# Kernel tuning notes

Measured on AMD Instinct MI355X. Metric: run time of the kernel, lower is better.

The kernel has to match this reference:

```python
import jax, jax.numpy as jnp
import numpy as np

B, OBS, D, V = 32, 768, 512, 64  # batch, obs_dim, latent/action/embed dim, max_vars


def _gelu(x):
    return jax.nn.gelu(x, approximate=False)  # torch nn.GELU default is exact erf


def setup_inputs() -> dict:
    key = jax.random.key(0)
    ks = jax.random.split(key, 16)
    s = lambda k, shape, scale=0.02: (jax.random.normal(k, shape, jnp.float32) * scale)
    return {
        "obs": jax.random.normal(ks[0], (B, OBS), jnp.float32),
        "action": jax.random.normal(ks[1], (B, D), jnp.float32),
        # CausalGraphLearner params
        "embed": jax.random.normal(ks[2], (V, D), jnp.float32),  # nn.Embedding weight
        "sc_w1": s(ks[3], (2 * D, 3 * D)), "sc_b1": jnp.zeros((2 * D,), jnp.float32),
        "sc_w2": s(ks[4], (1, 2 * D)), "sc_b2": jnp.zeros((1,), jnp.float32),
        # WorldModelEngine params
        "enc_w1": s(ks[5], (2 * D, OBS)), "enc_b1": jnp.zeros((2 * D,), jnp.float32),
        "enc_w2": s(ks[6], (D, 2 * D)), "enc_b2": jnp.zeros((D,), jnp.float32),
        "gru_wih": s(ks[7], (3 * D, 2 * D)), "gru_whh": s(ks[8], (3 * D, D)),
        "gru_bih": jnp.zeros((3 * D,), jnp.float32), "gru_bhh": jnp.zeros((3 * D,), jnp.float32),
        "dec_w": s(ks[9], (OBS, D)), "dec_b": jnp.zeros((OBS,), jnp.float32),
        # reasoner params
        "rs_w1": s(ks[10], (D, D)), "rs_b1": jnp.zeros((D,), jnp.float32),
        "rs_w2": s(ks[11], (D, D)), "rs_b2": jnp.zeros((D,), jnp.float32),
    }


def reference(obs, action, embed, sc_w1, sc_b1, sc_w2, sc_b2,
              enc_w1, enc_b1, enc_w2, enc_b2,
              gru_wih, gru_whh, gru_bih, gru_bhh,
              dec_w, dec_b, rs_w1, rs_b1, rs_w2, rs_b2):
    # --- WorldModelEngine ---
    z = _gelu(obs @ enc_w1.T + enc_b1) @ enc_w2.T + enc_b2            # [B, D]
    x = jnp.concatenate([z, action], axis=-1)                          # [B, 2D]
    h0 = jnp.zeros((obs.shape[0], D), obs.dtype)                       # h=None -> zeros
    gi = x @ gru_wih.T + gru_bih                                       # [B, 3D]
    gh = h0 @ gru_whh.T + gru_bhh                                      # [B, 3D]
    r = jax.nn.sigmoid(gi[:, :D] + gh[:, :D])
    u = jax.nn.sigmoid(gi[:, D:2 * D] + gh[:, D:2 * D])
    n = jnp.tanh(gi[:, 2 * D:] + r * gh[:, 2 * D:])
    h = (1.0 - u) * n + u * h0                                         # [B, D]
    pred = h @ dec_w.T + dec_b                                         # [B, OBS]

    # --- CausalGraphLearner ---
    # Linear-of-concat identity: W1 @ cat(cause, effect, ctx) = Wa@cause + Wb@effect + Wc@ctx
    Wa, Wb, Wc = sc_w1[:, :D], sc_w1[:, D:2 * D], sc_w1[:, 2 * D:]
    Ea = embed @ Wa.T                                                  # [V, 2D]
    Eb = embed @ Wb.T                                                  # [V, 2D]
    Cc = (h + action) @ Wc.T                                           # [B, 2D]
    hid = _gelu(Cc[:, None, None, :] + Ea[None, :, None, :]
                + Eb[None, None, :, :] + sc_b1)                        # [B, V, V, 2D]
    scores = jax.nn.sigmoid(jnp.einsum('bijd,d->bij', hid, sc_w2[0]) + sc_b2[0])  # [B,V,V]
    graph = scores.mean(0)                                             # [V, V] (returned scores)

    # --- reasoner ---
    reasoning = _gelu(h @ rs_w1.T + rs_b1) @ rs_w2.T + rs_b2           # [B, D]

    return (h, pred, graph, reasoning)
```

## Files before the change

### kernel.cpp

```cpp
#include <hip/hip_runtime.h>
#include <math.h>


#if __has_builtin(__builtin_amdgcn_exp2f)
#define EXP2F __builtin_amdgcn_exp2f
#else
#define EXP2F exp2f
#endif

typedef float f32x2 __attribute__((ext_vector_type(2)));

__device__ __forceinline__ float gelu_exact(float x) {
    return 0.5f * x * (1.f + erff(x * 0.70710678118654752f));
}
__device__ __forceinline__ float sigmoid_fast(float v) {
    return __builtin_amdgcn_rcpf(1.f + EXP2F(-1.442695041f * v));
}
__device__ __forceinline__ float tanh_fast(float v) {
    return fmaf(-2.f, __builtin_amdgcn_rcpf(1.f + EXP2F(2.885390082f * v)), 1.f);
}

template<int NF4, int ACT, int BT>
__device__ __forceinline__ void wgemm(int wid,
        const float* __restrict__ A, int lda,
        const float* __restrict__ W, int ldw,
        const float* __restrict__ bias,
        float* __restrict__ out, int ldo,
        int oblocks) {
    int lane = threadIdx.x & 63;
    int oblock = wid % oblocks;
    int bgroup = wid / oblocks;
    int o0 = oblock * 8, b0 = bgroup * BT;

    float4 w[8][NF4];
#pragma unroll
    for (int r = 0; r < 8; ++r) {
        const float4* wr = reinterpret_cast<const float4*>(W + (o0 + r) * ldw);
#pragma unroll
        for (int c = 0; c < NF4; ++c) w[r][c] = wr[c * 64 + lane];
    }
#pragma unroll 2
    for (int bi = 0; bi < BT; ++bi) {
        const float4* ar = reinterpret_cast<const float4*>(A + (b0 + bi) * lda);
        float4 a[NF4];
#pragma unroll
        for (int c = 0; c < NF4; ++c) a[c] = ar[c * 64 + lane];
        float s[8];
#pragma unroll
        for (int r = 0; r < 8; ++r) {
            float acc = 0.f;
#pragma unroll
            for (int c = 0; c < NF4; ++c) {
                acc = fmaf(a[c].x, w[r][c].x, acc);
                acc = fmaf(a[c].y, w[r][c].y, acc);
                acc = fmaf(a[c].z, w[r][c].z, acc);
                acc = fmaf(a[c].w, w[r][c].w, acc);
            }
            s[r] = acc;
        }
#pragma unroll
        for (int m = 1; m < 64; m <<= 1) {
#pragma unroll
            for (int r = 0; r < 8; ++r) s[r] += __shfl_xor(s[r], m, 64);
        }
        if (lane == 0) {
#pragma unroll
            for (int r = 0; r < 8; ++r) {
                float v = s[r] + (bias ? bias[o0 + r] : 0.f);
                if (ACT) v = gelu_exact(v);
                out[(b0 + bi) * ldo + o0 + r] = v;
            }
        }
    }
}

__global__ void __launch_bounds__(256) front_kernel(
    const float* __restrict__ obs, const float* __restrict__ enc_w1,
    const float* __restrict__ enc_b1, float* __restrict__ h1,
    const float* __restrict__ embed, const float* __restrict__ sc_w1,
    const float* __restrict__ sc_b1, float* __restrict__ Ea, float* __restrict__ Eb,
    const float* __restrict__ action, const float* __restrict__ wih,
    const float* __restrict__ bih, float* __restrict__ gia) {
    int wid = blockIdx.x * 4 + (threadIdx.x >> 6);
    if (wid < 512) {
        wgemm<3, 1, 8>(wid, obs, 768, enc_w1, 768, enc_b1, h1, 1024, 128);
    } else if (wid < 1536) {
        wgemm<2, 0, 8>(wid - 512, embed, 512, sc_w1, 1536, sc_b1, Ea, 1024, 128);
    } else if (wid < 2560) {
        wgemm<2, 0, 8>(wid - 1536, embed, 512, sc_w1 + 512, 1536, nullptr, Eb, 1024, 128);
    } else {
        wgemm<2, 0, 8>(wid - 2560, action, 512, wih + 512, 1024, bih, gia, 1536, 192);
    }
}

__global__ void __launch_bounds__(256) enc2_kernel(
    const float* __restrict__ h1, const float* __restrict__ enc_w2,
    const float* __restrict__ enc_b2, float* __restrict__ z) {
    int wid = blockIdx.x * 4 + (threadIdx.x >> 6);
    wgemm<4, 0, 4>(wid, h1, 1024, enc_w2, 1024, enc_b2, z, 512, 64);
}

__global__ void __launch_bounds__(256) gigru_kernel(
    const float* __restrict__ z, const float* __restrict__ wih,
    const float* __restrict__ gia, const float* __restrict__ bhh,
    const float* __restrict__ action, float* __restrict__ h, float* __restrict__ ha) {
    int wid = blockIdx.x * 4 + (threadIdx.x >> 6);
    int lane = threadIdx.x & 63;
    int opair = wid & 255;
    int bg = wid >> 8;
    int o0 = opair * 2, b0 = bg * 4;

    int rows[6] = {o0, o0 + 1, 512 + o0, 513 + o0, 1024 + o0, 1025 + o0};
    float4 w[6][2];
#pragma unroll
    for (int r = 0; r < 6; ++r) {
        const float4* wr = reinterpret_cast<const float4*>(wih + rows[r] * 1024);
#pragma unroll
        for (int c = 0; c < 2; ++c) w[r][c] = wr[c * 64 + lane];
    }
    float bhr0 = bhh[o0],        bhr1 = bhh[o0 + 1];
    float bhu0 = bhh[512 + o0],  bhu1 = bhh[513 + o0];
    float bhn0 = bhh[1024 + o0], bhn1 = bhh[1025 + o0];

#pragma unroll 2
    for (int bi = 0; bi < 4; ++bi) {
        int b = b0 + bi;
        const float4* ar = reinterpret_cast<const float4*>(z + b * 512);
        float4 a[2] = {ar[lane], ar[64 + lane]};
        float s[6];
#pragma unroll
        for (int r = 0; r < 6; ++r) {
            float acc = 0.f;
#pragma unroll
            for (int c = 0; c < 2; ++c) {
                acc = fmaf(a[c].x, w[r][c].x, acc);
                acc = fmaf(a[c].y, w[r][c].y, acc);
                acc = fmaf(a[c].z, w[r][c].z, acc);
                acc = fmaf(a[c].w, w[r][c].w, acc);
            }
            s[r] = acc;
        }
#pragma unroll
        for (int m = 1; m < 64; m <<= 1) {
#pragma unroll
            for (int r = 0; r < 6; ++r) s[r] += __shfl_xor(s[r], m, 64);
        }
        if (lane == 0) {
            const float* gb = gia + b * 1536;
            float r0 = sigmoid_fast(s[0] + gb[o0]        + bhr0);
            float r1 = sigmoid_fast(s[1] + gb[o0 + 1]    + bhr1);
            float u0 = sigmoid_fast(s[2] + gb[512 + o0]  + bhu0);
            float u1 = sigmoid_fast(s[3] + gb[513 + o0]  + bhu1);
            float n0 = tanh_fast(s[4] + gb[1024 + o0] + r0 * bhn0);
            float n1 = tanh_fast(s[5] + gb[1025 + o0] + r1 * bhn1);
            float hv0 = (1.f - u0) * n0;
            float hv1 = (1.f - u1) * n1;
            h[b * 512 + o0]      = hv0;
            h[b * 512 + o0 + 1]  = hv1;
            ha[b * 512 + o0]     = hv0 + action[b * 512 + o0];
            ha[b * 512 + o0 + 1] = hv1 + action[b * 512 + o0 + 1];
        }
    }
}

__global__ void __launch_bounds__(256) mid_kernel(
    const float* __restrict__ h, const float* __restrict__ ha,
    const float* __restrict__ dec_w, const float* __restrict__ dec_b, float* __restrict__ pred,
    const float* __restrict__ rs_w1, const float* __restrict__ rs_b1, float* __restrict__ r1,
    const float* __restrict__ sc_w1, float* __restrict__ Cc) {
    int wid = blockIdx.x * 4 + (threadIdx.x >> 6);
    if (wid < 768) {
        wgemm<2, 0, 4>(wid, h, 512, dec_w, 512, dec_b, pred, 768, 96);
    } else if (wid < 1280) {
        wgemm<2, 1, 4>(wid - 768, h, 512, rs_w1, 512, rs_b1, r1, 512, 64);
    } else {
        wgemm<2, 0, 4>(wid - 1280, ha, 512, sc_w1 + 1024, 1536, nullptr, Cc, 1024, 128);
    }
}

__global__ void __launch_bounds__(256) score_rs2_kernel(
    const float* __restrict__ Ea, const float* __restrict__ Eb,
    const float* __restrict__ Cc, const float* __restrict__ w2,
    const float* __restrict__ b2, float* __restrict__ graph,
    const float* __restrict__ r1, const float* __restrict__ rs_w2,
    const float* __restrict__ rs_b2, float* __restrict__ reasoning) {
    int blk = blockIdx.x;
    if (blk < 64) {
        int wid = blk * 4 + (threadIdx.x >> 6);
        wgemm<2, 0, 8>(wid, r1, 512, rs_w2, 512, rs_b2, reasoning, 512, 64);
    }
    int i = blk >> 5;
    int j0 = (blk & 31) << 1;
    int lane = threadIdx.x & 63;
    int wave = threadIdx.x >> 6;
    int d0 = lane << 4;

    const float4* Ea4  = reinterpret_cast<const float4*>(Ea + i * 1024 + d0);
    const float4* Eb04 = reinterpret_cast<const float4*>(Eb + j0 * 1024 + d0);
    const float4* Eb14 = reinterpret_cast<const float4*>(Eb + (j0 + 1) * 1024 + d0);
    const float4* W4   = reinterpret_cast<const float4*>(w2 + d0);

    f32x2 basea[8], baseb[8], wv[8];
#pragma unroll
    for (int c = 0; c < 4; ++c) {
        float4 e  = Ea4[c];
        float4 f0 = Eb04[c];
        float4 f1 = Eb14[c];
        float4 w  = W4[c];
        basea[2 * c]     = f32x2{e.x + f0.x, e.y + f0.y};
        basea[2 * c + 1] = f32x2{e.z + f0.z, e.w + f0.w};
        baseb[2 * c]     = f32x2{e.x + f1.x, e.y + f1.y};
        baseb[2 * c + 1] = f32x2{e.z + f1.z, e.w + f1.w};
        wv[2 * c]        = f32x2{w.x, w.y};
        wv[2 * c + 1]    = f32x2{w.z, w.w};
    }

    const f32x2 nk2  = f32x2{-2.4554274f, -2.4554274f};
    const f32x2 one2 = f32x2{1.f, 1.f};
    float bsc = b2[0];
    float gsum0 = 0.f, gsum1 = 0.f;
    const float4* p = reinterpret_cast<const float4*>(Cc + d0 + (wave * 8) * 1024);
    float4 m0 = p[0], m1 = p[1], m2 = p[2], m3 = p[3];

    for (int r = 0; r < 8; ++r) {
        f32x2 cc[8];
        cc[0] = f32x2{m0.x, m0.y}; cc[1] = f32x2{m0.z, m0.w};
        cc[2] = f32x2{m1.x, m1.y}; cc[3] = f32x2{m1.z, m1.w};
        cc[4] = f32x2{m2.x, m2.y}; cc[5] = f32x2{m2.z, m2.w};
        cc[6] = f32x2{m3.x, m3.y}; cc[7] = f32x2{m3.z, m3.w};
        if (r < 7) {
            const float4* q = reinterpret_cast<const float4*>(Cc + (wave * 8 + r + 1) * 1024 + d0);
            m0 = q[0]; m1 = q[1]; m2 = q[2]; m3 = q[3];
        }
        float s0 = 0.f, s1 = 0.f;
#pragma unroll
        for (int e = 0; e < 8; ++e) {
            f32x2 xA = cc[e] + basea[e];
            f32x2 xB = cc[e] + baseb[e];
            f32x2 aA = xA * nk2;
            f32x2 aB = xB * nk2;
            f32x2 tA, tB;
            tA.x = EXP2F(aA.x); tA.y = EXP2F(aA.y);
            tB.x = EXP2F(aB.x); tB.y = EXP2F(aB.y);
            f32x2 dA = tA + one2;
            f32x2 dB = tB + one2;
            f32x2 pA = xA * wv[e];
            f32x2 pB = xB * wv[e];
            float numA = fmaf(pA.x, dA.y, pA.y * dA.x);
            float numB = fmaf(pB.x, dB.y, pB.y * dB.x);
            float rrA = __builtin_amdgcn_rcpf(dA.x * dA.y);
            float rrB = __builtin_amdgcn_rcpf(dB.x * dB.y);
            s0 = fmaf(numA, rrA, s0);
            s1 = fmaf(numB, rrB, s1);
        }
#pragma unroll
        for (int m = 32; m >= 1; m >>= 1) {
            s0 += __shfl_xor(s0, m, 64);
            s1 += __shfl_xor(s1, m, 64);
        }
        if (lane == 0) {
            gsum0 += sigmoid_fast(s0 + bsc);
            gsum1 += sigmoid_fast(s1 + bsc);
        }
    }

    __shared__ float red[4][2];
    if (lane == 0) { red[wave][0] = gsum0; red[wave][1] = gsum1; }
    __syncthreads();
    if (threadIdx.x == 0) {
        graph[i * 64 + j0]     = (red[0][0] + red[1][0] + red[2][0] + red[3][0]) * 0.03125f;
        graph[i * 64 + j0 + 1] = (red[0][1] + red[1][1] + red[2][1] + red[3][1]) * 0.03125f;
    }
}

extern "C" void kernel_launch(void* const* d_in, const int* in_sizes, int n_in,
                              void* d_out, int out_size, void* d_ws, size_t ws_size,
                              hipStream_t stream) {
    const float* obs     = (const float*)d_in[0];
    const float* action  = (const float*)d_in[1];
    const float* embed   = (const float*)d_in[2];
    const float* sc_w1   = (const float*)d_in[3];
    const float* sc_b1   = (const float*)d_in[4];
    const float* sc_w2   = (const float*)d_in[5];
    const float* sc_b2   = (const float*)d_in[6];
    const float* enc_w1  = (const float*)d_in[7];
    const float* enc_b1  = (const float*)d_in[8];
    const float* enc_w2  = (const float*)d_in[9];
    const float* enc_b2  = (const float*)d_in[10];
    const float* gru_wih = (const float*)d_in[11];
    const float* gru_bih = (const float*)d_in[13];
    const float* gru_bhh = (const float*)d_in[14];
    const float* dec_w   = (const float*)d_in[15];
    const float* dec_b   = (const float*)d_in[16];
    const float* rs_w1   = (const float*)d_in[17];
    const float* rs_b1   = (const float*)d_in[18];
    const float* rs_w2   = (const float*)d_in[19];
    const float* rs_b2   = (const float*)d_in[20];

    float* ws = (float*)d_ws;
    float* h1  = ws + 0;
    float* z   = ws + 32768;
    float* gia = ws + 49152;
    float* ha  = ws + 98304;
    float* r1  = ws + 114688;
    float* Cc  = ws + 131072;
    float* Ea  = ws + 163840;
    float* Eb  = ws + 229376;

    float* h_out     = (float*)d_out;
    float* pred      = h_out + 16384;
    float* graph     = h_out + 40960;
    float* reasoning = h_out + 45056;

    front_kernel<<<832, 256, 0, stream>>>(obs, enc_w1, enc_b1, h1,
                                          embed, sc_w1, sc_b1, Ea, Eb,
                                          action, gru_wih, gru_bih, gia);
    enc2_kernel<<<128, 256, 0, stream>>>(h1, enc_w2, enc_b2, z);
    gigru_kernel<<<512, 256, 0, stream>>>(z, gru_wih, gia, gru_bhh, action, h_out, ha);
    mid_kernel<<<576, 256, 0, stream>>>(h_out, ha, dec_w, dec_b, pred,
                                        rs_w1, rs_b1, r1, sc_w1, Cc);
    score_rs2_kernel<<<2048, 256, 0, stream>>>(Ea, Eb, Cc, sc_w2, sc_b2, graph,
                                               r1, rs_w2, rs_b2, reasoning);
}
```

Measured before the change: 198.9 us.

## Use transpose-style shuffle reductions and halve batch tiles for more waves

The wave-level reductions in the GEMV helper and the score kernel now use a butterfly that folds several partial sums per shuffle step. This replaces independent full 64-lane reductions for each output and cuts the number of cross-lane shuffles. The score kernel now accumulates all 8 batch rows before a single combined reduction, instead of reducing once per row. The enc2, GRU and mid kernels use half the batch rows per wave with twice as many blocks, trading more weight reloads for more parallelism.

```diff
diff --git a/kernel.cpp b/kernel.cpp
--- a/kernel.cpp
+++ b/kernel.cpp
@@ -7,8 +7,6 @@
 #else
 #define EXP2F exp2f
 #endif
-
-typedef float f32x2 __attribute__((ext_vector_type(2)));
 
 __device__ __forceinline__ float gelu_exact(float x) {
     return 0.5f * x * (1.f + erff(x * 0.70710678118654752f));
@@ -39,7 +37,10 @@
 #pragma unroll
         for (int c = 0; c < NF4; ++c) w[r][c] = wr[c * 64 + lane];
     }
-#pragma unroll 2
+    float bv = bias ? bias[o0 + (lane & 7)] : 0.f;
+    bool p0 = lane & 1, p1 = lane & 2, p2 = lane & 4;
+
+#pragma unroll
     for (int bi = 0; bi < BT; ++bi) {
         const float4* ar = reinterpret_cast<const float4*>(A + (b0 + bi) * lda);
         float4 a[NF4];
@@ -58,19 +59,32 @@
             }
             s[r] = acc;
         }
-#pragma unroll
-        for (int m = 1; m < 64; m <<= 1) {
-#pragma unroll
-            for (int r = 0; r < 8; ++r) s[r] += __shfl_xor(s[r], m, 64);
-        }
-        if (lane == 0) {
-#pragma unroll
-            for (int r = 0; r < 8; ++r) {
-                float v = s[r] + (bias ? bias[o0 + r] : 0.f);
-                if (ACT) v = gelu_exact(v);
-                out[(b0 + bi) * ldo + o0 + r] = v;
-            }
-        }
+        float m[4];
+#pragma unroll
+        for (int k = 0; k < 4; ++k) {
+            float keep = p0 ? s[2 * k + 1] : s[2 * k];
+            float send = p0 ? s[2 * k] : s[2 * k + 1];
+            m[k] = keep + __shfl_xor(send, 1, 64);
+        }
+        float n[2];
+#pragma unroll
+        for (int k = 0; k < 2; ++k) {
+            float keep = p1 ? m[2 * k + 1] : m[2 * k];
+            float send = p1 ? m[2 * k] : m[2 * k + 1];
+            n[k] = keep + __shfl_xor(send, 2, 64);
+        }
+        float F;
+        {
+            float keep = p2 ? n[1] : n[0];
+            float send = p2 ? n[0] : n[1];
+            F = keep + __shfl_xor(send, 4, 64);
+        }
+        F += __shfl_xor(F, 8, 64);
+        F += __shfl_xor(F, 16, 64);
+        F += __shfl_xor(F, 32, 64);
+        float v = F + bv;
+        if (ACT) v = gelu_exact(v);
+        if (lane < 8) out[(b0 + bi) * ldo + o0 + lane] = v;
     }
 }
 
@@ -97,7 +111,7 @@
     const float* __restrict__ h1, const float* __restrict__ enc_w2,
     const float* __restrict__ enc_b2, float* __restrict__ z) {
     int wid = blockIdx.x * 4 + (threadIdx.x >> 6);
-    wgemm<4, 0, 4>(wid, h1, 1024, enc_w2, 1024, enc_b2, z, 512, 64);
+    wgemm<4, 0, 2>(wid, h1, 1024, enc_w2, 1024, enc_b2, z, 512, 64);
 }
 
 __global__ void __launch_bounds__(256) gigru_kernel(
@@ -108,7 +122,7 @@
     int lane = threadIdx.x & 63;
     int opair = wid & 255;
     int bg = wid >> 8;
-    int o0 = opair * 2, b0 = bg * 4;
+    int o0 = opair * 2, b0 = bg * 2;
 
     int rows[6] = {o0, o0 + 1, 512 + o0, 513 + o0, 1024 + o0, 1025 + o0};
     float4 w[6][2];
@@ -122,8 +136,8 @@
     float bhu0 = bhh[512 + o0],  bhu1 = bhh[513 + o0];
     float bhn0 = bhh[1024 + o0], bhn1 = bhh[1025 + o0];
 
-#pragma unroll 2
-    for (int bi = 0; bi < 4; ++bi) {
+#pragma unroll
+    for (int bi = 0; bi < 2; ++bi) {
         int b = b0 + bi;
         const float4* ar = reinterpret_cast<const float4*>(z + b * 512);
         float4 a[2] = {ar[lane], ar[64 + lane]};
@@ -169,12 +183,12 @@
     const float* __restrict__ rs_w1, const float* __restrict__ rs_b1, float* __restrict__ r1,
     const float* __restrict__ sc_w1, float* __restrict__ Cc) {
     int wid = blockIdx.x * 4 + (threadIdx.x >> 6);
-    if (wid < 768) {
-        wgemm<2, 0, 4>(wid, h, 512, dec_w, 512, dec_b, pred, 768, 96);
-    } else if (wid < 1280) {
-        wgemm<2, 1, 4>(wid - 768, h, 512, rs_w1, 512, rs_b1, r1, 512, 64);
+    if (wid < 1536) {
+        wgemm<2, 0, 2>(wid, h, 512, dec_w, 512, dec_b, pred, 768, 96);
+    } else if (wid < 2560) {
+        wgemm<2, 1, 2>(wid - 1536, h, 512, rs_w1, 512, rs_b1, r1, 512, 64);
     } else {
-        wgemm<2, 0, 4>(wid - 1280, ha, 512, sc_w1 + 1024, 1536, nullptr, Cc, 1024, 128);
+        wgemm<2, 0, 2>(wid - 2560, ha, 512, sc_w1 + 1024, 1536, nullptr, Cc, 1024, 128);
     }
 }
 
@@ -200,76 +214,96 @@
     const float4* Eb14 = reinterpret_cast<const float4*>(Eb + (j0 + 1) * 1024 + d0);
     const float4* W4   = reinterpret_cast<const float4*>(w2 + d0);
 
-    f32x2 basea[8], baseb[8], wv[8];
+    float basea[16], baseb[16], wv[16];
 #pragma unroll
     for (int c = 0; c < 4; ++c) {
         float4 e  = Ea4[c];
         float4 f0 = Eb04[c];
         float4 f1 = Eb14[c];
         float4 w  = W4[c];
-        basea[2 * c]     = f32x2{e.x + f0.x, e.y + f0.y};
-        basea[2 * c + 1] = f32x2{e.z + f0.z, e.w + f0.w};
-        baseb[2 * c]     = f32x2{e.x + f1.x, e.y + f1.y};
-        baseb[2 * c + 1] = f32x2{e.z + f1.z, e.w + f1.w};
-        wv[2 * c]        = f32x2{w.x, w.y};
-        wv[2 * c + 1]    = f32x2{w.z, w.w};
-    }
-
-    const f32x2 nk2  = f32x2{-2.4554274f, -2.4554274f};
-    const f32x2 one2 = f32x2{1.f, 1.f};
-    float bsc = b2[0];
-    float gsum0 = 0.f, gsum1 = 0.f;
-    const float4* p = reinterpret_cast<const float4*>(Cc + d0 + (wave * 8) * 1024);
-    float4 m0 = p[0], m1 = p[1], m2 = p[2], m3 = p[3];
-
-    for (int r = 0; r < 8; ++r) {
-        f32x2 cc[8];
-        cc[0] = f32x2{m0.x, m0.y}; cc[1] = f32x2{m0.z, m0.w};
-        cc[2] = f32x2{m1.x, m1.y}; cc[3] = f32x2{m1.z, m1.w};
-        cc[4] = f32x2{m2.x, m2.y}; cc[5] = f32x2{m2.z, m2.w};
-        cc[6] = f32x2{m3.x, m3.y}; cc[7] = f32x2{m3.z, m3.w};
-        if (r < 7) {
-            const float4* q = reinterpret_cast<const float4*>(Cc + (wave * 8 + r + 1) * 1024 + d0);
-            m0 = q[0]; m1 = q[1]; m2 = q[2]; m3 = q[3];
-        }
-        float s0 = 0.f, s1 = 0.f;
-#pragma unroll
-        for (int e = 0; e < 8; ++e) {
-            f32x2 xA = cc[e] + basea[e];
-            f32x2 xB = cc[e] + baseb[e];
-            f32x2 aA = xA * nk2;
-            f32x2 aB = xB * nk2;
-            f32x2 tA, tB;
-            tA.x = EXP2F(aA.x); tA.y = EXP2F(aA.y);
-            tB.x = EXP2F(aB.x); tB.y = EXP2F(aB.y);
-            f32x2 dA = tA + one2;
-            f32x2 dB = tB + one2;
-            f32x2 pA = xA * wv[e];
-            f32x2 pB = xB * wv[e];
-            float numA = fmaf(pA.x, dA.y, pA.y * dA.x);
-            float numB = fmaf(pB.x, dB.y, pB.y * dB.x);
-            float rrA = __builtin_amdgcn_rcpf(dA.x * dA.y);
-            float rrB = __builtin_amdgcn_rcpf(dB.x * dB.y);
-            s0 = fmaf(numA, rrA, s0);
-            s1 = fmaf(numB, rrB, s1);
-        }
-#pragma unroll
-        for (int m = 32; m >= 1; m >>= 1) {
-            s0 += __shfl_xor(s0, m, 64);
-            s1 += __shfl_xor(s1, m, 64);
-        }
-        if (lane == 0) {
-            gsum0 += sigmoid_fast(s0 + bsc);
-            gsum1 += sigmoid_fast(s1 + bsc);
-        }
-    }
+        basea[4 * c + 0] = e.x + f0.x; basea[4 * c + 1] = e.y + f0.y;
+        basea[4 * c + 2] = e.z + f0.z; basea[4 * c + 3] = e.w + f0.w;
+        baseb[4 * c + 0] = e.x + f1.x; baseb[4 * c + 1] = e.y + f1.y;
+        baseb[4 * c + 2] = e.z + f1.z; baseb[4 * c + 3] = e.w + f1.w;
+        wv[4 * c + 0] = w.x; wv[4 * c + 1] = w.y;
+        wv[4 * c + 2] = w.z; wv[4 * c + 3] = w.w;
+    }
+
+    const float NK = -2.4554274f;
+    float sA[8], sB[8];
+#pragma unroll
+    for (int b = 0; b < 8; ++b) { sA[b] = 0.f; sB[b] = 0.f; }
+
+    const float* ccbase = Cc + (wave * 8) * 1024 + d0;
+#pragma unroll
+    for (int b = 0; b < 8; ++b) {
+        const float4* q = reinterpret_cast<const float4*>(ccbase + b * 1024);
+        float4 c0 = q[0], c1 = q[1], c2 = q[2], c3 = q[3];
+        float cc[16] = {c0.x, c0.y, c0.z, c0.w, c1.x, c1.y, c1.z, c1.w,
+                        c2.x, c2.y, c2.z, c2.w, c3.x, c3.y, c3.z, c3.w};
+#pragma unroll
+        for (int e = 0; e < 16; e += 2) {
+            float xa0 = cc[e] + basea[e];
+            float xa1 = cc[e + 1] + basea[e + 1];
+            float ta0 = EXP2F(xa0 * NK);
+            float ta1 = EXP2F(xa1 * NK);
+            float da0 = 1.f + ta0, da1 = 1.f + ta1;
+            float numa = fmaf(xa0 * wv[e], da1, (xa1 * wv[e + 1]) * da0);
+            sA[b] = fmaf(numa, __builtin_amdgcn_rcpf(da0 * da1), sA[b]);
+
+            float xb0 = cc[e] + baseb[e];
+            float xb1 = cc[e + 1] + baseb[e + 1];
+            float tb0 = EXP2F(xb0 * NK);
+            float tb1 = EXP2F(xb1 * NK);
+            float db0 = 1.f + tb0, db1 = 1.f + tb1;
+            float numb = fmaf(xb0 * wv[e], db1, (xb1 * wv[e + 1]) * db0);
+            sB[b] = fmaf(numb, __builtin_amdgcn_rcpf(db0 * db1), sB[b]);
+        }
+    }
+
+    bool p0 = lane & 1, p1 = lane & 2, p2 = lane & 4, p3 = lane & 8;
+    float m[8];
+#pragma unroll
+    for (int k = 0; k < 8; ++k) {
+        float keep = p0 ? sB[k] : sA[k];
+        float send = p0 ? sA[k] : sB[k];
+        m[k] = keep + __shfl_xor(send, 1, 64);
+    }
+    float n[4];
+#pragma unroll
+    for (int k = 0; k < 4; ++k) {
+        float keep = p1 ? m[2 * k + 1] : m[2 * k];
+        float send = p1 ? m[2 * k] : m[2 * k + 1];
+        n[k] = keep + __shfl_xor(send, 2, 64);
+    }
+    float o2[2];
+#pragma unroll
+    for (int k = 0; k < 2; ++k) {
+        float keep = p2 ? n[2 * k + 1] : n[2 * k];
+        float send = p2 ? n[2 * k] : n[2 * k + 1];
+        o2[k] = keep + __shfl_xor(send, 4, 64);
+    }
+    float F;
+    {
+        float keep = p3 ? o2[1] : o2[0];
+        float send = p3 ? o2[0] : o2[1];
+        F = keep + __shfl_xor(send, 8, 64);
+    }
+    F += __shfl_xor(F, 16, 64);
+    F += __shfl_xor(F, 32, 64);
+
+    float sig = sigmoid_fast(F + b2[0]);
+    sig += __shfl_xor(sig, 2, 64);
+    sig += __shfl_xor(sig, 4, 64);
+    sig += __shfl_xor(sig, 8, 64);
 
     __shared__ float red[4][2];
-    if (lane == 0) { red[wave][0] = gsum0; red[wave][1] = gsum1; }
+    if (lane < 2) red[wave][lane] = sig;
     __syncthreads();
-    if (threadIdx.x == 0) {
-        graph[i * 64 + j0]     = (red[0][0] + red[1][0] + red[2][0] + red[3][0]) * 0.03125f;
-        graph[i * 64 + j0 + 1] = (red[0][1] + red[1][1] + red[2][1] + red[3][1]) * 0.03125f;
+    if (threadIdx.x < 2) {
+        graph[i * 64 + j0 + threadIdx.x] =
+            (red[0][threadIdx.x] + red[1][threadIdx.x] +
+             red[2][threadIdx.x] + red[3][threadIdx.x]) * 0.03125f;
     }
 }
 
@@ -315,10 +349,10 @@
     front_kernel<<<832, 256, 0, stream>>>(obs, enc_w1, enc_b1, h1,
                                           embed, sc_w1, sc_b1, Ea, Eb,
                                           action, gru_wih, gru_bih, gia);
-    enc2_kernel<<<128, 256, 0, stream>>>(h1, enc_w2, enc_b2, z);
-    gigru_kernel<<<512, 256, 0, stream>>>(z, gru_wih, gia, gru_bhh, action, h_out, ha);
-    mid_kernel<<<576, 256, 0, stream>>>(h_out, ha, dec_w, dec_b, pred,
-                                        rs_w1, rs_b1, r1, sc_w1, Cc);
+    enc2_kernel<<<256, 256, 0, stream>>>(h1, enc_w2, enc_b2, z);
+    gigru_kernel<<<1024, 256, 0, stream>>>(z, gru_wih, gia, gru_bhh, action, h_out, ha);
+    mid_kernel<<<1152, 256, 0, stream>>>(h_out, ha, dec_w, dec_b, pred,
+                                         rs_w1, rs_b1, r1, sc_w1, Cc);
     score_rs2_kernel<<<2048, 256, 0, stream>>>(Ea, Eb, Cc, sc_w2, sc_b2, graph,
                                                r1, rs_w2, rs_b2, reasoning);
 }
```

Result: faster. 172.8 us (-13.1%).
